# Optimization experiments

Measured on AMD Instinct MI355X. Metric: run time of the kernel, lower is better.

Reference implementation:

```python
import jax, jax.numpy as jnp
import numpy as np


def setup_inputs() -> dict:
    key = jax.random.key(0)
    k1, k2 = jax.random.split(key)
    imgs = jax.random.normal(k1, (16, 64, 64, 64), dtype=jnp.float32)
    # matches np.random.normal(0, 0.01, (1, inCs, outCs, filtSize, filtSize, 2))
    filts = 0.01 * jax.random.normal(k2, (1, 64, 64, 3, 3, 2), dtype=jnp.float32)
    return {"imgs": imgs, "filts": filts}


def reference(imgs, filts):
    # imgs:  [B, inC, H, W] real
    # filts: [1, inC, outC, fs, fs, 2] (real/imag planes)
    B, inC, H, W = imgs.shape
    fs = filts.shape[3]
    # zero-pad image to S = H + fs - 1 (full linear-conv FFT size)
    imgs_p = jnp.pad(imgs, ((0, 0), (0, 0), (0, fs - 1), (0, fs - 1)))
    img_f = jnp.fft.fftn(imgs_p, axes=(-2, -1))  # [B, inC, S, S] complex64
    # complex filter, padded to same FFT size
    fc = (filts[0, ..., 0] + 1j * filts[0, ..., 1]).astype(jnp.complex64)  # [inC, outC, fs, fs]
    fc_p = jnp.pad(fc, ((0, 0), (0, 0), (0, H - 1), (0, W - 1)))
    filt_f = jnp.fft.fftn(fc_p, axes=(-2, -1))  # [inC, outC, S, S]
    # Karatsuba complex multiply + sum over inC == complex contraction over inC.
    # Fused as one einsum instead of materializing [B,inC,outC,S,S] intermediates.
    out_f = jnp.einsum('bihw,iohw->bohw', img_f, filt_f)  # [B, outC, S, S]
    out = jnp.fft.ifftn(out_f, axes=(-2, -1))
    # crop [1:-1, 1:-1] and take real part, as in the torch module
    return out[:, :, 1:-1, 1:-1].real.astype(imgs.dtype)
```

## Files before the change

### kernel.cpp

```cpp
#include <hip/hip_runtime.h>


typedef _Float16 f16x8 __attribute__((ext_vector_type(8)));
typedef float    f32x4 __attribute__((ext_vector_type(4)));

#define NB 16
#define NC 64
#define NH 64
#define NW 64
#define CHUNKS 528
#define SLAB_BYTES (CHUNKS * 16)
#define WF_HALFS (9 * 2 * 4 * 64 * 8)

__global__ __launch_bounds__(256) void prep_w(const float* __restrict__ filts,
                                              _Float16* __restrict__ wf) {
    const int f = blockIdx.x * 256 + threadIdx.x;
    if (f >= WF_HALFS) return;
    const int e  = f & 7;
    const int l  = (f >> 3) & 63;
    const int n  = (f >> 9) & 3;
    const int kc = (f >> 11) & 1;
    const int t  = f >> 12;
    const int i  = kc * 32 + (l >> 4) * 8 + e;
    const int o  = n * 16 + (l & 15);
    const int ky = t / 3, kx = t % 3;
    wf[f] = (_Float16)filts[(((i * 64 + o) * 3 + ky) * 3 + kx) * 2];
}

__global__ __launch_bounds__(256, 2) void conv_direct(const float* __restrict__ imgs,
                                                      const _Float16* __restrict__ wf,
                                                      float* __restrict__ out) {
    __shared__ uint4 ldsb[4 * SLAB_BYTES / 16];
    char* lds = reinterpret_cast<char*>(ldsb);
    const int bid = blockIdx.x;
    const int swz = ((bid & 7) << 6) | (bid >> 3);
    const int b   = swz >> 5;
    const int y0  = (swz & 31) << 1;
    const int tid = threadIdx.x;
    const int w   = tid >> 6;
    const int l   = tid & 63;
    const int h   = l >> 4;
    const int r   = l & 15;

    {
        const int rs = w;
        const int y  = y0 + rs - 1;
        const bool yv = ((unsigned)y < (unsigned)NH);
        char* slab = lds + rs * SLAB_BYTES;
        #pragma unroll
        for (int ci = 0; ci < 8; ++ci) {
            f16x8 v;
            if (yv) {
                const float* src = imgs + (((size_t)(b * NC + ci * 8)) * NH + y) * NW + l;
                #pragma unroll
                for (int k = 0; k < 8; ++k) v[k] = (_Float16)src[(size_t)k * NH * NW];
            } else {
                #pragma unroll
                for (int k = 0; k < 8; ++k) v[k] = (_Float16)0.f;
            }
            const int xp = l + 1;
            const int chunk = xp * 8 + (ci ^ (xp & 7));
            *reinterpret_cast<f16x8*>(slab + chunk * 16) = v;
            if (l < 2) {
                const int xp2 = l ? 65 : 0;
                const int c2  = xp2 * 8 + (ci ^ (xp2 & 7));
                f16x8 z;
                #pragma unroll
                for (int k = 0; k < 8; ++k) z[k] = (_Float16)0.f;
                *reinterpret_cast<f16x8*>(slab + c2 * 16) = z;
            }
        }
    }
    __syncthreads();

    const int row = w >> 1;
    const int oh  = w & 1;

    f32x4 acc[4][2];
    #pragma unroll
    for (int m = 0; m < 4; ++m)
        #pragma unroll
        for (int n = 0; n < 2; ++n)
            acc[m][n] = f32x4{0.f, 0.f, 0.f, 0.f};

    #pragma unroll
    for (int ky = 0; ky < 3; ++ky) {
        const char* slab = lds + (row + 2 - ky) * SLAB_BYTES;
        #pragma unroll
        for (int kx = 0; kx < 3; ++kx) {
            const _Float16* wft = wf + (size_t)(ky * 3 + kx) * (2 * 4 * 64 * 8);
            #pragma unroll
            for (int kc = 0; kc < 2; ++kc) {
                f16x8 a[4], bb[2];
                #pragma unroll
                for (int m = 0; m < 4; ++m) {
                    const int xp = m * 16 + r + 2 - kx;
                    const int chunk = xp * 8 + (((kc << 2) + h) ^ (xp & 7));
                    a[m] = *reinterpret_cast<const f16x8*>(slab + chunk * 16);
                }
                #pragma unroll
                for (int n = 0; n < 2; ++n)
                    bb[n] = *reinterpret_cast<const f16x8*>(
                        wft + ((size_t)((kc << 2) + (oh * 2 + n)) * 64 + l) * 8);
                #pragma unroll
                for (int m = 0; m < 4; ++m)
                    #pragma unroll
                    for (int n = 0; n < 2; ++n)
                        acc[m][n] = __builtin_amdgcn_mfma_f32_16x16x32_f16(a[m], bb[n], acc[m][n], 0, 0, 0);
            }
        }
    }

    const int y = y0 + row;
    #pragma unroll
    for (int m = 0; m < 4; ++m) {
        const int x0 = m * 16 + h * 4;
        #pragma unroll
        for (int n = 0; n < 2; ++n) {
            const int o = oh * 32 + n * 16 + r;
            *reinterpret_cast<f32x4*>(out + (((size_t)(b * 64 + o) * 64 + y) * 64) + x0) = acc[m][n];
        }
    }
}

extern "C" void kernel_launch(void* const* d_in, const int* in_sizes, int n_in,
                              void* d_out, int out_size, void* d_ws, size_t ws_size,
                              hipStream_t stream) {
    const float* imgs  = (const float*)d_in[0];
    const float* filts = (const float*)d_in[1];
    float* out = (float*)d_out;
    _Float16* wfb = (_Float16*)d_ws;

    hipLaunchKernelGGL(prep_w, dim3((WF_HALFS + 255) / 256), dim3(256), 0, stream, filts, wfb);
    hipLaunchKernelGGL(conv_direct, dim3(NB * 32), dim3(256), 0, stream, imgs, wfb, out);
}
```

Baseline: 21.24 us.

## Pre-convert images to padded fp16 slabs and stage them via global_load_lds

Adds a prep pass that converts the fp32 image into zero-padded, swizzled fp16 row slabs in workspace, merged into one launch with the weight repack. The conv kernel then fills LDS with direct global-to-LDS 16-byte loads instead of strided fp32 gathers and in-kernel conversion. This is meant to cut the long-latency scattered loads in the conv kernel. In exchange it adds an extra workspace write and read of the image, and each 9 KB slab copy reads slightly past the 8448-byte row into the next row.

```diff
diff --git a/kernel.cpp b/kernel.cpp
--- a/kernel.cpp
+++ b/kernel.cpp
@@ -2,6 +2,7 @@
 
 
 typedef _Float16 f16x8 __attribute__((ext_vector_type(8)));
+typedef __fp16   fp16x2 __attribute__((ext_vector_type(2)));
 typedef float    f32x4 __attribute__((ext_vector_type(4)));
 
 #define NB 16
@@ -10,28 +11,77 @@
 #define NW 64
 #define CHUNKS 528
 #define SLAB_BYTES (CHUNKS * 16)
+#define SLAB_HALFS (CHUNKS * 8)
+#define LDS_SLAB 9216
+#define PIMG_ROWS (NB * 66 + 1)
 #define WF_HALFS (9 * 2 * 4 * 64 * 8)
 
-__global__ __launch_bounds__(256) void prep_w(const float* __restrict__ filts,
-                                              _Float16* __restrict__ wf) {
-    const int f = blockIdx.x * 256 + threadIdx.x;
-    if (f >= WF_HALFS) return;
-    const int e  = f & 7;
-    const int l  = (f >> 3) & 63;
-    const int n  = (f >> 9) & 3;
-    const int kc = (f >> 11) & 1;
-    const int t  = f >> 12;
-    const int i  = kc * 32 + (l >> 4) * 8 + e;
-    const int o  = n * 16 + (l & 15);
-    const int ky = t / 3, kx = t % 3;
-    wf[f] = (_Float16)filts[(((i * 64 + o) * 3 + ky) * 3 + kx) * 2];
+typedef __attribute__((address_space(3))) unsigned int lds_u32;
+typedef __attribute__((address_space(1))) const unsigned int gbl_u32;
+
+__global__ __launch_bounds__(256) void prep(const float* __restrict__ imgs,
+                                            const float* __restrict__ filts,
+                                            _Float16* __restrict__ pimg,
+                                            _Float16* __restrict__ wf) {
+    const int bid = blockIdx.x;
+    const int tid = threadIdx.x;
+    if (bid < NB * 66) {
+        const int b  = bid / 66;
+        const int yp = bid % 66;
+        char* row = (char*)(pimg + (size_t)bid * SLAB_HALFS);
+        if (yp == 0 || yp == 65) {
+            f16x8 z;
+            #pragma unroll
+            for (int k = 0; k < 8; ++k) z[k] = (_Float16)0.f;
+            for (int c = tid; c < CHUNKS; c += 256)
+                *reinterpret_cast<f16x8*>(row + c * 16) = z;
+            return;
+        }
+        const int y = yp - 1;
+        const int w = tid >> 6;
+        const int l = tid & 63;
+        if (tid < 16) {
+            const int ci  = tid >> 1;
+            const int xpp = (tid & 1) ? 65 : 0;
+            const int c2  = xpp * 8 + (ci ^ (xpp & 7));
+            f16x8 z;
+            #pragma unroll
+            for (int k = 0; k < 8; ++k) z[k] = (_Float16)0.f;
+            *reinterpret_cast<f16x8*>(row + c2 * 16) = z;
+        }
+        float f[16];
+        const float* src = imgs + ((size_t)(b * NC + w * 16)) * NH * NW + (size_t)y * NW + l;
+        #pragma unroll
+        for (int k = 0; k < 16; ++k) f[k] = src[(size_t)k * NH * NW];
+        const int xp = l + 1;
+        #pragma unroll
+        for (int j = 0; j < 2; ++j) {
+            const int ci = w * 2 + j;
+            union { f16x8 v; fp16x2 h2[4]; } u;
+            #pragma unroll
+            for (int p = 0; p < 4; ++p)
+                u.h2[p] = __builtin_amdgcn_cvt_pkrtz(f[j * 8 + 2 * p], f[j * 8 + 2 * p + 1]);
+            const int chunk = xp * 8 + (ci ^ (xp & 7));
+            *reinterpret_cast<f16x8*>(row + chunk * 16) = u.v;
+        }
+    } else {
+        const int f = (bid - NB * 66) * 256 + tid;
+        const int e  = f & 7;
+        const int l  = (f >> 3) & 63;
+        const int n  = (f >> 9) & 3;
+        const int kc = (f >> 11) & 1;
+        const int t  = f >> 12;
+        const int i  = kc * 32 + (l >> 4) * 8 + e;
+        const int o  = n * 16 + (l & 15);
+        const int ky = t / 3, kx = t % 3;
+        wf[f] = (_Float16)filts[(((i * 64 + o) * 3 + ky) * 3 + kx) * 2];
+    }
 }
 
-__global__ __launch_bounds__(256, 2) void conv_direct(const float* __restrict__ imgs,
-                                                      const _Float16* __restrict__ wf,
-                                                      float* __restrict__ out) {
-    __shared__ uint4 ldsb[4 * SLAB_BYTES / 16];
-    char* lds = reinterpret_cast<char*>(ldsb);
+__global__ __launch_bounds__(256, 2) void conv(const _Float16* __restrict__ pimg,
+                                               const _Float16* __restrict__ wf,
+                                               float* __restrict__ out) {
+    __shared__ char lds[4 * LDS_SLAB];
     const int bid = blockIdx.x;
     const int swz = ((bid & 7) << 6) | (bid >> 3);
     const int b   = swz >> 5;
@@ -43,32 +93,13 @@
     const int r   = l & 15;
 
     {
-        const int rs = w;
-        const int y  = y0 + rs - 1;
-        const bool yv = ((unsigned)y < (unsigned)NH);
-        char* slab = lds + rs * SLAB_BYTES;
+        const char* g = (const char*)(pimg + (size_t)(b * 66 + y0 + w) * SLAB_HALFS);
+        char* d = lds + w * LDS_SLAB;
         #pragma unroll
-        for (int ci = 0; ci < 8; ++ci) {
-            f16x8 v;
-            if (yv) {
-                const float* src = imgs + (((size_t)(b * NC + ci * 8)) * NH + y) * NW + l;
-                #pragma unroll
-                for (int k = 0; k < 8; ++k) v[k] = (_Float16)src[(size_t)k * NH * NW];
-            } else {
-                #pragma unroll
-                for (int k = 0; k < 8; ++k) v[k] = (_Float16)0.f;
-            }
-            const int xp = l + 1;
-            const int chunk = xp * 8 + (ci ^ (xp & 7));
-            *reinterpret_cast<f16x8*>(slab + chunk * 16) = v;
-            if (l < 2) {
-                const int xp2 = l ? 65 : 0;
-                const int c2  = xp2 * 8 + (ci ^ (xp2 & 7));
-                f16x8 z;
-                #pragma unroll
-                for (int k = 0; k < 8; ++k) z[k] = (_Float16)0.f;
-                *reinterpret_cast<f16x8*>(slab + c2 * 16) = z;
-            }
+        for (int k = 0; k < 9; ++k) {
+            __builtin_amdgcn_global_load_lds(
+                (gbl_u32*)(g + k * 1024 + l * 16),
+                (lds_u32*)(d + k * 1024), 16, 0, 0);
         }
     }
     __syncthreads();
@@ -85,7 +116,7 @@
 
     #pragma unroll
     for (int ky = 0; ky < 3; ++ky) {
-        const char* slab = lds + (row + 2 - ky) * SLAB_BYTES;
+        const char* slab = lds + (row + 2 - ky) * LDS_SLAB;
         #pragma unroll
         for (int kx = 0; kx < 3; ++kx) {
             const _Float16* wft = wf + (size_t)(ky * 3 + kx) * (2 * 4 * 64 * 8);
@@ -129,8 +160,11 @@
     const float* imgs  = (const float*)d_in[0];
     const float* filts = (const float*)d_in[1];
     float* out = (float*)d_out;
-    _Float16* wfb = (_Float16*)d_ws;
 
-    hipLaunchKernelGGL(prep_w, dim3((WF_HALFS + 255) / 256), dim3(256), 0, stream, filts, wfb);
-    hipLaunchKernelGGL(conv_direct, dim3(NB * 32), dim3(256), 0, stream, imgs, wfb, out);
+    _Float16* pimg = (_Float16*)d_ws;
+    _Float16* wfb  = pimg + (size_t)PIMG_ROWS * SLAB_HALFS;
+
+    hipLaunchKernelGGL(prep, dim3(NB * 66 + WF_HALFS / 256), dim3(256), 0, stream,
+                       imgs, filts, pimg, wfb);
+    hipLaunchKernelGGL(conv, dim3(NB * 32), dim3(256), 0, stream, pimg, wfb, out);
 }
```

Measured after the change: 23.98 us. 1.13x slower.
